# Kernel tuning notes

Measured on AMD Instinct MI355X. Metric: run time of the kernel, lower is better.

## Reference

```python
import jax, jax.numpy as jnp
import numpy as np

B, S, E, CS, NC, H = 4, 2048, 1024, 16, 8, 16
D = E + CS            # d_model = 1040
DH = D // H           # head_dim = 65
DFF = 4 * E           # forward_expansion * embed_size


def setup_inputs() -> dict:
    key = jax.random.key(0)
    ks = jax.random.split(key, 20)
    s = 0.02  # init scale for weights
    f32 = jnp.float32
    return {
        'x': jax.random.normal(ks[0], (B, S, E), f32),
        'conditioning': jax.random.uniform(ks[1], (B, S, CS), f32),
        # attention params (torch Linear convention: W is [out, in])
        'Wq': jax.random.normal(ks[2], (D, D), f32) * s,
        'bq': jnp.zeros((D,), f32),
        'Wv': jax.random.normal(ks[3], (D, D), f32) * s,
        'bv': jnp.zeros((D,), f32),
        'Wk': jax.random.normal(ks[4], (NC, D, D), f32) * s,  # stacked per-class key projections
        'bk': jnp.zeros((NC, D), f32),
        'Wo': jax.random.normal(ks[5], (D, D), f32) * s,
        'bo': jnp.zeros((D,), f32),
        # layernorms
        'g1': jnp.ones((E,), f32), 'bn1': jnp.zeros((E,), f32),
        'g2': jnp.ones((E,), f32), 'bn2': jnp.zeros((E,), f32),
        # feed-forward
        'Wf1': jax.random.normal(ks[6], (DFF, E), f32) * s,
        'bf1': jnp.zeros((DFF,), f32),
        'Wf2': jax.random.normal(ks[7], (E, DFF), f32) * s,
        'bf2': jnp.zeros((E,), f32),
    }


def _layernorm(x, g, b, eps=1e-5):
    m = jnp.mean(x, axis=-1, keepdims=True)
    v = jnp.mean(jnp.square(x - m), axis=-1, keepdims=True)
    return (x - m) * jax.lax.rsqrt(v + eps) * g + b


def reference(x, conditioning, Wq, bq, Wv, bv, Wk, bk, Wo, bo,
              g1, bn1, g2, bn2, Wf1, bf1, Wf2, bf2):
    # dropout is identity (eval mode)
    xn = _layernorm(x, g1, bn1)                       # [B,S,E]
    xc = jnp.concatenate([xn, conditioning], axis=-1)  # [B,S,D]

    q = (xc @ Wq.T + bq).reshape(B, S, H, DH).transpose(0, 2, 1, 3)  # [B,H,S,DH]
    v = (xc @ Wv.T + bv).reshape(B, S, H, DH).transpose(0, 2, 1, 3)

    # per-class keys: [B,C,S,D], then weighted-sum by conditioning[:,:,:NC]
    keys = jnp.einsum('bsd,cod->bcso', xc, Wk) + bk[None, :, None, :]
    w = conditioning[:, :, :NC]                        # [B,S,C]
    k = jnp.einsum('bsc,bcso->bso', w, keys)           # [B,S,D]
    k = k.reshape(B, S, H, DH).transpose(0, 2, 1, 3)   # [B,H,S,DH]

    scale = 1.0 / np.sqrt(DH).astype(np.float32)
    scores = jnp.einsum('bhqd,bhkd->bhqk', q, k) * scale
    attn = jax.nn.softmax(scores, axis=-1)
    o = jnp.einsum('bhqk,bhkd->bhqd', attn, v)
    o = o.transpose(0, 2, 1, 3).reshape(B, S, D)
    o = o @ Wo.T + bo

    h = xn + o[:, :, :E]                               # residual uses normed x
    ff = jnp.maximum(h @ Wf1.T + bf1, 0.0) @ Wf2.T + bf2
    return _layernorm(h + ff, g2, bn2)
```

## Files before the change

kernel.cpp:

```cpp
#include <hip/hip_runtime.h>
#include <hip/hip_bf16.h>
#include <math.h>

typedef __bf16 bf16;
typedef __bf16 v8bf __attribute__((ext_vector_type(8)));
typedef float v4f __attribute__((ext_vector_type(4)));

#define B_   4
#define S_   2048
#define E_   1024
#define CS_  16
#define NC_  8
#define H_   16
#define D_   1040
#define DH_  65
#define DFF_ 4096
#define M_   8192
#define KC_  1056
#define KH_  (4 * KC_)
#define KB2_ (8 * KC_)

__device__ __forceinline__ v4f mfma16(v8bf a, v8bf b, v4f c) {
    return __builtin_amdgcn_mfma_f32_16x16x32_bf16(a, b, c, 0, 0, 0);
}

__device__ __forceinline__ void async16(const bf16* g, bf16* l) {
    __builtin_amdgcn_global_load_lds(
        (const __attribute__((address_space(1))) unsigned int*)g,
        (__attribute__((address_space(3))) unsigned int*)l, 16, 0, 0);
}

__global__ __launch_bounds__(256) void k_cvt(const float* __restrict__ src,
                                             bf16* __restrict__ dst, int n) {
    int i = (blockIdx.x * 256 + threadIdx.x) * 4;
    if (i + 4 <= n) {
        float4 v = *(const float4*)(src + i);
        bf16 o[4] = {(bf16)v.x, (bf16)v.y, (bf16)v.z, (bf16)v.w};
        *(ushort4*)(dst + i) = *(const ushort4*)o;
    }
}

__global__ __launch_bounds__(256) void k_build_bk(const float* __restrict__ Wk,
                                                  bf16* __restrict__ Bp) {
    int c = blockIdx.y;
    int idx = blockIdx.x * 256 + threadIdx.x;
    if (idx >= 1040 * 130) return;
    int n = idx / 130, u = idx - n * 130;
    const float* src = Wk + ((size_t)(c * D_ + n)) * D_ + u * 8;
    float4 a = *(const float4*)src;
    float4 b = *(const float4*)(src + 4);
    bf16 o[8] = {(bf16)a.x, (bf16)a.y, (bf16)a.z, (bf16)a.w,
                 (bf16)b.x, (bf16)b.y, (bf16)b.z, (bf16)b.w};
    *(uint4*)(Bp + (size_t)n * KB2_ + c * KC_ + u * 8) = *(const uint4*)o;
}

__global__ __launch_bounds__(256) void k_scale_a(const bf16* __restrict__ xc,
                                                 const float* __restrict__ cond,
                                                 int coff, bf16* __restrict__ Ap) {
    int idx = blockIdx.x * 256 + threadIdx.x;
    int m = idx / 132, u = idx - m * 132;
    int j = u * 8;
    float4 w4 = *(const float4*)(cond + (size_t)m * CS_ + coff);
    float wv[4] = {w4.x, w4.y, w4.z, w4.w};
    bf16* dst = Ap + (size_t)m * KH_ + j;
    if (j < D_) {
        union { uint4 u4; bf16 h[8]; } src;
        src.u4 = *(const uint4*)(xc + (size_t)m * D_ + j);
        float xv[8];
#pragma unroll
        for (int e = 0; e < 8; ++e) xv[e] = (float)src.h[e];
#pragma unroll
        for (int cc = 0; cc < 4; ++cc) {
            bf16 o[8];
#pragma unroll
            for (int e = 0; e < 8; ++e) o[e] = (bf16)(xv[e] * wv[cc]);
            *(uint4*)(dst + cc * KC_) = *(const uint4*)o;
        }
    } else {
        uint4 z = {0u, 0u, 0u, 0u};
#pragma unroll
        for (int cc = 0; cc < 4; ++cc) *(uint4*)(dst + cc * KC_) = z;
    }
}

__global__ __launch_bounds__(256) void k_zero_pads(bf16* __restrict__ qp,
                                                   bf16* __restrict__ kp) {
    int i = blockIdx.x * 256 + threadIdx.x;
    int row = i >> 3, j = i & 7;
    uint4 z = {0u, 0u, 0u, 0u};
    bf16* base = (j < 4) ? qp : kp;
    ((uint4*)(base + (size_t)row * 96 + 64))[j & 3] = z;
}

__global__ __launch_bounds__(256) void k_ln_concat(
    const float* __restrict__ x, const float* __restrict__ cond,
    const float* __restrict__ g, const float* __restrict__ bn,
    bf16* __restrict__ xc)
{
    int row = blockIdx.x;
    int t = threadIdx.x;
    const float* xr = x + (size_t)row * E_;
    float4 v = *(const float4*)(xr + t * 4);
    float s = v.x + v.y + v.z + v.w;
    float ss = v.x * v.x + v.y * v.y + v.z * v.z + v.w * v.w;
#pragma unroll
    for (int off = 32; off; off >>= 1) {
        s  += __shfl_down(s, off);
        ss += __shfl_down(ss, off);
    }
    __shared__ float red[8];
    int wid = t >> 6;
    if ((t & 63) == 0) { red[wid] = s; red[4 + wid] = ss; }
    __syncthreads();
    float stot  = red[0] + red[1] + red[2] + red[3];
    float sstot = red[4] + red[5] + red[6] + red[7];
    float mean = stot * (1.0f / E_);
    float var  = sstot * (1.0f / E_) - mean * mean;
    float rs = rsqrtf(var + 1e-5f);
    bf16* xcr = xc + (size_t)row * D_;
    float vv[4] = {v.x, v.y, v.z, v.w};
#pragma unroll
    for (int j = 0; j < 4; ++j) {
        int i = t * 4 + j;
        xcr[i] = (bf16)(((vv[j] - mean) * rs) * g[i] + bn[i]);
    }
    if (t < CS_) xcr[E_ + t] = (bf16)cond[(size_t)row * CS_ + t];
}

__global__ __launch_bounds__(256) void k_gemm_k2(
    const bf16* __restrict__ A, const bf16* __restrict__ Bm,
    int koffB, bf16* __restrict__ Pout)
{
    __shared__ bf16 As[128][32];
    __shared__ bf16 Bs[128][32];
    int t = threadIdx.x;

    int pid = blockIdx.x;
    int gid = pid / 72;
    int rem = pid - gid * 72;
    int mi = gid * 8 + (rem & 7);
    int ni = rem >> 3;
    int m0 = mi << 7, n0 = ni << 7;

    int lane = t & 63, w = t >> 6;
    int wm = (w >> 1) * 64, wn = (w & 1) * 64;
    int lr = lane & 15, lq = lane >> 4;

    int row_i[2], seg_i[2];
#pragma unroll
    for (int i = 0; i < 2; ++i) { row_i[i] = (t + i * 256) >> 2; seg_i[i] = (t + i * 256) & 3; }

    v4f acc[4][4];
    v4f vzero = {0.f, 0.f, 0.f, 0.f};
#pragma unroll
    for (int mt = 0; mt < 4; ++mt)
#pragma unroll
        for (int nt = 0; nt < 4; ++nt) acc[mt][nt] = vzero;

    for (int kb = 0; kb < KH_ / 32; ++kb) {
        int k0 = kb << 5;
#pragma unroll
        for (int i = 0; i < 2; ++i) {
            async16(A + (size_t)(m0 + row_i[i]) * KH_ + k0 + seg_i[i] * 8,
                    &As[0][0] + (t + i * 256) * 8);
            async16(Bm + (size_t)(n0 + row_i[i]) * KB2_ + koffB + k0 + seg_i[i] * 8,
                    &Bs[0][0] + (t + i * 256) * 8);
        }
        __syncthreads();
        v8bf af[4], bfr[4];
#pragma unroll
        for (int mt = 0; mt < 4; ++mt) af[mt]  = *(const v8bf*)(&As[wm + mt * 16 + lr][lq * 8]);
#pragma unroll
        for (int nt = 0; nt < 4; ++nt) bfr[nt] = *(const v8bf*)(&Bs[wn + nt * 16 + lr][lq * 8]);
#pragma unroll
        for (int mt = 0; mt < 4; ++mt)
#pragma unroll
            for (int nt = 0; nt < 4; ++nt)
                acc[mt][nt] = mfma16(af[mt], bfr[nt], acc[mt][nt]);
        __syncthreads();
    }

#pragma unroll
    for (int mt = 0; mt < 4; ++mt)
#pragma unroll
        for (int reg = 0; reg < 4; ++reg) {
            int grow = m0 + wm + mt * 16 + lq * 4 + reg;
#pragma unroll
            for (int nt = 0; nt < 4; ++nt) {
                int gcol = n0 + wn + nt * 16 + lr;
                if (gcol < D_)
                    Pout[(size_t)grow * D_ + gcol] = (bf16)acc[mt][nt][reg];
            }
        }
}

__global__ __launch_bounds__(256) void k_comb_k(
    const bf16* __restrict__ P0, const bf16* __restrict__ P1,
    const float* __restrict__ condw, const float* __restrict__ bkp,
    bf16* __restrict__ kp)
{
    int idx = blockIdx.x * 256 + threadIdx.x;
    int m = idx / 1040, n = idx - m * 1040;
    float v = (float)P0[idx] + (float)P1[idx];
#pragma unroll
    for (int c = 0; c < NC_; ++c)
        v += condw[(size_t)m * CS_ + c] * bkp[(size_t)c * D_ + n];
    int h = n / 65, d = n - h * 65;
    int b = m >> 11, s = m & 2047;
    kp[(((size_t)(b * 16 + h)) * S_ + s) * 96 + d] = (bf16)v;
}

#define EP_QV  0
#define EP_O   1
#define EP_FF1 2
#define EP_FF2 3

template<int EP>
__global__ __launch_bounds__(256) void k_gemm(
    const bf16* __restrict__ A, const bf16* __restrict__ Bm,
    const float* __restrict__ bias, const float* __restrict__ bias2,
    int M, int N, int K, int lda, int ldb, int nbn,
    bf16* __restrict__ Cb, float* __restrict__ Cf, int ldc,
    const bf16* __restrict__ res, int ldres, bf16* __restrict__ Cb2)
{
    __shared__ bf16 As[128][32];
    __shared__ bf16 Bs[128][32];
    int t = threadIdx.x;

    int pid = blockIdx.x;
    int nig = 8 * nbn;
    int gid = pid / nig;
    int rem = pid - gid * nig;
    int mi = gid * 8 + (rem & 7);
    int ni = rem >> 3;
    int m0 = mi << 7, n0 = ni << 7;

    int lane = t & 63, w = t >> 6;
    int wm = (w >> 1) * 64, wn = (w & 1) * 64;
    int lr = lane & 15, lq = lane >> 4;

    int row_i[2], seg_i[2];
#pragma unroll
    for (int i = 0; i < 2; ++i) { row_i[i] = (t + i * 256) >> 2; seg_i[i] = (t + i * 256) & 3; }

    v4f acc[4][4];
    v4f vzero = {0.f, 0.f, 0.f, 0.f};
#pragma unroll
    for (int mt = 0; mt < 4; ++mt)
#pragma unroll
        for (int nt = 0; nt < 4; ++nt) acc[mt][nt] = vzero;

    const int KF = K >> 5;
    const bool KR = (K & 31) != 0;

    for (int kb = 0; kb < KF; ++kb) {
        int k0 = kb << 5;
#pragma unroll
        for (int i = 0; i < 2; ++i) {
            async16(A + (size_t)(m0 + row_i[i]) * lda + k0 + seg_i[i] * 8,
                    &As[0][0] + (t + i * 256) * 8);
            async16(Bm + (size_t)(n0 + row_i[i]) * ldb + k0 + seg_i[i] * 8,
                    &Bs[0][0] + (t + i * 256) * 8);
        }
        __syncthreads();
        v8bf af[4], bfr[4];
#pragma unroll
        for (int mt = 0; mt < 4; ++mt) af[mt]  = *(const v8bf*)(&As[wm + mt * 16 + lr][lq * 8]);
#pragma unroll
        for (int nt = 0; nt < 4; ++nt) bfr[nt] = *(const v8bf*)(&Bs[wn + nt * 16 + lr][lq * 8]);
#pragma unroll
        for (int mt = 0; mt < 4; ++mt)
#pragma unroll
            for (int nt = 0; nt < 4; ++nt)
                acc[mt][nt] = mfma16(af[mt], bfr[nt], acc[mt][nt]);
        __syncthreads();
    }
    if (KR) {
        int k0 = KF << 5;
#pragma unroll
        for (int i = 0; i < 2; ++i) {
            int gk = k0 + seg_i[i] * 8;
            uint4 val = {0u, 0u, 0u, 0u};
            if (gk + 8 <= K) val = *(const uint4*)(A + (size_t)(m0 + row_i[i]) * lda + gk);
            *(uint4*)(&As[row_i[i]][seg_i[i] * 8]) = val;
            uint4 bv = {0u, 0u, 0u, 0u};
            int gn = n0 + row_i[i];
            if (gn < N && gk + 8 <= K) bv = *(const uint4*)(Bm + (size_t)gn * ldb + gk);
            *(uint4*)(&Bs[row_i[i]][seg_i[i] * 8]) = bv;
        }
        __syncthreads();
        v8bf af[4], bfr[4];
#pragma unroll
        for (int mt = 0; mt < 4; ++mt) af[mt]  = *(const v8bf*)(&As[wm + mt * 16 + lr][lq * 8]);
#pragma unroll
        for (int nt = 0; nt < 4; ++nt) bfr[nt] = *(const v8bf*)(&Bs[wn + nt * 16 + lr][lq * 8]);
#pragma unroll
        for (int mt = 0; mt < 4; ++mt)
#pragma unroll
            for (int nt = 0; nt < 4; ++nt)
                acc[mt][nt] = mfma16(af[mt], bfr[nt], acc[mt][nt]);
        __syncthreads();
    }

#pragma unroll
    for (int mt = 0; mt < 4; ++mt) {
#pragma unroll
        for (int reg = 0; reg < 4; ++reg) {
            int grow = m0 + wm + mt * 16 + lq * 4 + reg;
#pragma unroll
            for (int nt = 0; nt < 4; ++nt) {
                int gcol = n0 + wn + nt * 16 + lr;
                float vacc = acc[mt][nt][reg];
                if constexpr (EP == EP_QV) {
                    if (gcol < D_) {
                        float o = (vacc + bias[gcol]) * 0.1789442960f;
                        int h = gcol / 65, d = gcol - h * 65;
                        int b = grow >> 11, s = grow & 2047;
                        Cb[(((size_t)(b * 16 + h)) * S_ + s) * 96 + d] = (bf16)o;
                    } else if (gcol < 2 * D_) {
                        int col = gcol - D_;
                        Cb2[(size_t)grow * D_ + col] = (bf16)(vacc + bias2[col]);
                    }
                } else if constexpr (EP == EP_O) {
                    float o = vacc + bias[gcol] + (float)res[(size_t)grow * ldres + gcol];
                    Cb[(size_t)grow * ldc + gcol] = (bf16)o;
                } else if constexpr (EP == EP_FF1) {
                    float o = vacc + bias[gcol];
                    Cb[(size_t)grow * ldc + gcol] = (bf16)fmaxf(o, 0.f);
                } else {
                    Cf[(size_t)grow * ldc + gcol] =
                        vacc + bias[gcol] + (float)res[(size_t)grow * ldres + gcol];
                }
            }
        }
    }
}

__global__ __launch_bounds__(256) void k_transpose_v(
    const bf16* __restrict__ v, bf16* __restrict__ vt)
{
    int bh = blockIdx.y, s0 = blockIdx.x * 64;
    int b = bh >> 4, h = bh & 15;
    __shared__ bf16 tile[80][65];
#pragma unroll
    for (int i = 0; i < 20; ++i) {
        int idx = threadIdx.x + i * 256;
        int d = idx % 80, sl = idx / 80;
        bf16 val = (bf16)0.f;
        if (d < DH_) val = v[((size_t)b * S_ + s0 + sl) * D_ + h * DH_ + d];
        tile[d][sl] = val;
    }
    __syncthreads();
#pragma unroll
    for (int i = 0; i < 20; ++i) {
        int idx = threadIdx.x + i * 256;
        int sl = idx % 64, d = idx / 64;
        vt[((size_t)bh * 80 + d) * S_ + s0 + sl] = tile[d][sl];
    }
}

__global__ __launch_bounds__(256) void k_attn(
    const bf16* __restrict__ qp, const bf16* __restrict__ kp,
    const bf16* __restrict__ vt, bf16* __restrict__ o)
{
    int bh = blockIdx.y;
    int s0 = blockIdx.x * 64;
    int b = bh >> 4, h = bh & 15;
    int t = threadIdx.x, lane = t & 63, w = t >> 6;
    int lr = lane & 15, lq = lane >> 4;

    __shared__ bf16 Kbuf[2][64 * 96];
    __shared__ bf16 Psh[4][16 * 72];
    bf16* Ps = Psh[w];
    bf16* k0p = &Kbuf[0][0];

    const bf16* qbase = qp + ((size_t)bh * S_ + s0 + w * 16 + lr) * 96;
    v8bf qreg[3];
#pragma unroll
    for (int ks = 0; ks < 3; ++ks)
        qreg[ks] = *(const v8bf*)(qbase + ks * 32 + lq * 8);

    const bf16* kpb = kp + (size_t)bh * S_ * 96;
    const bf16* vbase = vt + ((size_t)bh * 80 + lr) * S_ + lq * 8;

#pragma unroll
    for (int i = 0; i < 3; ++i)
        async16(kpb + (t + i * 256) * 8, k0p + (t + i * 256) * 8);

    float m_s = -1e30f, l_s = 0.f;
    v4f o_acc[5];
    v4f vzero = {0.f, 0.f, 0.f, 0.f};
#pragma unroll
    for (int nt = 0; nt < 5; ++nt) o_acc[nt] = vzero;

    __syncthreads();

    int cur = 0;
    for (int kb = 0; kb < S_ / 64; ++kb) {
        const bf16* Kc = k0p + cur * (64 * 96);
        if (kb + 1 < S_ / 64) {
            bf16* Kn = k0p + (cur ^ 1) * (64 * 96);
            const bf16* src = kpb + (size_t)(kb + 1) * (64 * 96);
#pragma unroll
            for (int i = 0; i < 3; ++i)
                async16(src + (t + i * 256) * 8, Kn + (t + i * 256) * 8);
        }

        v4f sacc[4];
#pragma unroll
        for (int kt = 0; kt < 4; ++kt) sacc[kt] = vzero;
        __builtin_amdgcn_s_setprio(1);
#pragma unroll
        for (int ks = 0; ks < 3; ++ks)
#pragma unroll
            for (int kt = 0; kt < 4; ++kt) {
                v8bf kf = *(const v8bf*)(Kc + (kt * 16 + lr) * 96 + ks * 32 + lq * 8);
                sacc[kt] = mfma16(kf, qreg[ks], sacc[kt]);
            }
        __builtin_amdgcn_s_setprio(0);

        v8bf vf0[5], vf1[5];
        const bf16* vb0 = vbase + kb * 64;
#pragma unroll
        for (int nt = 0; nt < 5; ++nt) vf0[nt] = *(const v8bf*)(vb0 + nt * 16 * S_);
#pragma unroll
        for (int nt = 0; nt < 5; ++nt) vf1[nt] = *(const v8bf*)(vb0 + nt * 16 * S_ + 32);

        float mx = sacc[0][0];
#pragma unroll
        for (int kt = 0; kt < 4; ++kt)
#pragma unroll
            for (int r = 0; r < 4; ++r) mx = fmaxf(mx, sacc[kt][r]);
        mx = fmaxf(mx, __shfl_xor(mx, 16));
        mx = fmaxf(mx, __shfl_xor(mx, 32));
        float mnew = fmaxf(m_s, mx);
        float alpha = __builtin_amdgcn_exp2f(m_s - mnew);
        float ps = 0.f;
#pragma unroll
        for (int kt = 0; kt < 4; ++kt) {
            bf16 p4[4];
#pragma unroll
            for (int r = 0; r < 4; ++r) {
                float p = __builtin_amdgcn_exp2f(sacc[kt][r] - mnew);
                ps += p;
                p4[r] = (bf16)p;
            }
            *(uint2*)(&Ps[lr * 72 + kt * 16 + lq * 4]) = *(const uint2*)p4;
        }
        ps += __shfl_xor(ps, 16);
        ps += __shfl_xor(ps, 32);
        l_s = l_s * alpha + ps;
        m_s = mnew;

#pragma unroll
        for (int nt = 0; nt < 5; ++nt)
#pragma unroll
            for (int r = 0; r < 4; ++r) o_acc[nt][r] *= alpha;

        asm volatile("s_waitcnt lgkmcnt(0)" ::: "memory");

        __builtin_amdgcn_s_setprio(1);
        {
            v8bf pf0 = *(const v8bf*)(&Ps[lr * 72 + lq * 8]);
            v8bf pf1 = *(const v8bf*)(&Ps[lr * 72 + 32 + lq * 8]);
#pragma unroll
            for (int nt = 0; nt < 5; ++nt) o_acc[nt] = mfma16(vf0[nt], pf0, o_acc[nt]);
#pragma unroll
            for (int nt = 0; nt < 5; ++nt) o_acc[nt] = mfma16(vf1[nt], pf1, o_acc[nt]);
        }
        __builtin_amdgcn_s_setprio(0);
        __syncthreads();
        cur ^= 1;
    }

    float inv = 1.0f / l_s;
    bf16* obase = o + (size_t)(b * S_ + s0 + w * 16 + lr) * D_ + h * DH_;
#pragma unroll
    for (int nt = 0; nt < 4; ++nt)
#pragma unroll
        for (int r = 0; r < 4; ++r)
            obase[nt * 16 + lq * 4 + r] = (bf16)(o_acc[nt][r] * inv);
    if (lq == 0) obase[64] = (bf16)(o_acc[4][0] * inv);
}

__global__ __launch_bounds__(256) void k_ln_out(
    const float* __restrict__ z, const float* __restrict__ g,
    const float* __restrict__ bn, float* __restrict__ out)
{
    int row = blockIdx.x;
    int t = threadIdx.x;
    const float* zr = z + (size_t)row * E_;
    float4 v = *(const float4*)(zr + t * 4);
    float s = v.x + v.y + v.z + v.w;
    float ss = v.x * v.x + v.y * v.y + v.z * v.z + v.w * v.w;
#pragma unroll
    for (int off = 32; off; off >>= 1) {
        s  += __shfl_down(s, off);
        ss += __shfl_down(ss, off);
    }
    __shared__ float red[8];
    int wid = t >> 6;
    if ((t & 63) == 0) { red[wid] = s; red[4 + wid] = ss; }
    __syncthreads();
    float stot  = red[0] + red[1] + red[2] + red[3];
    float sstot = red[4] + red[5] + red[6] + red[7];
    float mean = stot * (1.0f / E_);
    float var  = sstot * (1.0f / E_) - mean * mean;
    float rs = rsqrtf(var + 1e-5f);
    float* outr = out + (size_t)row * E_;
    float vv[4] = {v.x, v.y, v.z, v.w};
#pragma unroll
    for (int j = 0; j < 4; ++j) {
        int i = t * 4 + j;
        outr[i] = ((vv[j] - mean) * rs) * g[i] + bn[i];
    }
}

extern "C" void kernel_launch(void* const* d_in, const int* in_sizes, int n_in,
                              void* d_out, int out_size, void* d_ws, size_t ws_size,
                              hipStream_t stream) {
    const float* x    = (const float*)d_in[0];
    const float* cond = (const float*)d_in[1];
    const float* Wq   = (const float*)d_in[2];
    const float* bq   = (const float*)d_in[3];
    const float* Wv   = (const float*)d_in[4];
    const float* bv   = (const float*)d_in[5];
    const float* Wk   = (const float*)d_in[6];
    const float* bk   = (const float*)d_in[7];
    const float* Wo   = (const float*)d_in[8];
    const float* bo   = (const float*)d_in[9];
    const float* g1   = (const float*)d_in[10];
    const float* bn1  = (const float*)d_in[11];
    const float* g2   = (const float*)d_in[12];
    const float* bn2  = (const float*)d_in[13];
    const float* Wf1  = (const float*)d_in[14];
    const float* bf1  = (const float*)d_in[15];
    const float* Wf2  = (const float*)d_in[16];
    const float* bf2  = (const float*)d_in[17];
    float* out = (float*)d_out;

    char* ws = (char*)d_ws;
    bf16* Wqv_b = (bf16*)(ws + 0);
    bf16* Wo_b  = (bf16*)(ws + 4526080);
    bf16* Wf1_b = (bf16*)(ws + 6656000);
    bf16* Wf2_b = (bf16*)(ws + 15044608);
    bf16*  xc   = (bf16*)(ws + 23433216);
    bf16*  Bpk  = (bf16*)(ws + 40472576);
    bf16*  Apk  = (bf16*)(ws + 59936768);
    bf16*  P0k  = (bf16*)(ws + 129142784);
    bf16*  P1k  = (bf16*)(ws + 146182144);
    bf16*  qp   = (bf16*)(ws + 40472576);
    bf16*  kp   = (bf16*)(ws + 65638400);
    bf16*  vb   = (bf16*)(ws + 90804224);
    bf16*  hb   = (bf16*)(ws + 90804224);
    bf16*  vtb  = (bf16*)(ws + 107843584);
    bf16*  ob   = (bf16*)(ws + 128815104);
    bf16*  ff1  = (bf16*)(ws + 23433216);
    float* zb   = (float*)(ws + 107843584);

    k_cvt<<<(1081600 / 4 + 255) / 256, 256, 0, stream>>>(Wq, Wqv_b, 1081600);
    k_cvt<<<(1081600 / 4 + 255) / 256, 256, 0, stream>>>(Wv, Wqv_b + 1081600, 1081600);
    k_cvt<<<(1064960 / 4 + 255) / 256, 256, 0, stream>>>(Wo, Wo_b, 1064960);
    k_cvt<<<(4194304 / 4 + 255) / 256, 256, 0, stream>>>(Wf1, Wf1_b, 4194304);
    k_cvt<<<(4194304 / 4 + 255) / 256, 256, 0, stream>>>(Wf2, Wf2_b, 4194304);

    k_ln_concat<<<M_, 256, 0, stream>>>(x, cond, g1, bn1, xc);

    k_build_bk<<<dim3((1040 * 130 + 255) / 256, 8), 256, 0, stream>>>(Wk, Bpk);
    k_scale_a<<<(M_ * 132) / 256, 256, 0, stream>>>(xc, cond, 0, Apk);
    k_gemm_k2<<<576, 256, 0, stream>>>(Apk, Bpk, 0, P0k);
    k_scale_a<<<(M_ * 132) / 256, 256, 0, stream>>>(xc, cond, 4, Apk);
    k_gemm_k2<<<576, 256, 0, stream>>>(Apk, Bpk, KH_, P1k);

    k_zero_pads<<<4096, 256, 0, stream>>>(qp, kp);
    k_comb_k<<<(M_ * D_) / 256, 256, 0, stream>>>(P0k, P1k, cond, bk, kp);

    k_gemm<EP_QV><<<64 * 17, 256, 0, stream>>>(xc, Wqv_b, bq, bv, M_, 2 * D_, D_, D_, D_, 17,
                                               qp, nullptr, 0, nullptr, 0, vb);

    k_transpose_v<<<dim3(S_ / 64, 64), 256, 0, stream>>>(vb, vtb);
    k_attn<<<dim3(S_ / 64, 64), 256, 0, stream>>>(qp, kp, vtb, ob);

    k_gemm<EP_O><<<64 * 8, 256, 0, stream>>>(ob, Wo_b, bo, nullptr, M_, E_, D_, D_, D_, 8,
                                             hb, nullptr, E_, xc, D_, nullptr);
    k_gemm<EP_FF1><<<64 * 32, 256, 0, stream>>>(hb, Wf1_b, bf1, nullptr, M_, DFF_, E_, E_, E_, 32,
                                                ff1, nullptr, DFF_, nullptr, 0, nullptr);
    k_gemm<EP_FF2><<<64 * 8, 256, 0, stream>>>(ff1, Wf2_b, bf2, nullptr, M_, E_, DFF_, DFF_, DFF_, 8,
                                               nullptr, zb, E_, hb, E_, nullptr);

    k_ln_out<<<M_, 256, 0, stream>>>(zb, g2, bn2, out);
}
```

Measured before the change: 1.123 ms.

## Process two query tiles per attention block, stage V in LDS with XOR swizzle

Measured after the change: 958.9 us. 14.6% less time.

```diff
diff --git a/kernel.cpp b/kernel.cpp
--- a/kernel.cpp
+++ b/kernel.cpp
@@ -207,7 +207,8 @@
         v += condw[(size_t)m * CS_ + c] * bkp[(size_t)c * D_ + n];
     int h = n / 65, d = n - h * 65;
     int b = m >> 11, s = m & 2047;
-    kp[(((size_t)(b * 16 + h)) * S_ + s) * 96 + d] = (bf16)v;
+    int d2 = (d < 64) ? (d ^ ((s & 7) << 3)) : (d ^ ((s & 3) << 3));
+    kp[(((size_t)(b * 16 + h)) * S_ + s) * 96 + d2] = (bf16)v;
 }
 
 #define EP_QV  0
@@ -355,7 +356,8 @@
     for (int i = 0; i < 20; ++i) {
         int idx = threadIdx.x + i * 256;
         int sl = idx % 64, d = idx / 64;
-        vt[((size_t)bh * 80 + d) * S_ + s0 + sl] = tile[d][sl];
+        int sl2 = sl ^ ((d & 7) << 3);
+        vt[((size_t)bh * 80 + d) * S_ + s0 + sl2] = tile[d][sl];
     }
 }
 
@@ -364,123 +366,185 @@
     const bf16* __restrict__ vt, bf16* __restrict__ o)
 {
     int bh = blockIdx.y;
-    int s0 = blockIdx.x * 64;
+    int s0 = blockIdx.x * 128;
     int b = bh >> 4, h = bh & 15;
     int t = threadIdx.x, lane = t & 63, w = t >> 6;
     int lr = lane & 15, lq = lane >> 4;
 
     __shared__ bf16 Kbuf[2][64 * 96];
+    __shared__ bf16 Vbuf[2][80 * 64];
     __shared__ bf16 Psh[4][16 * 72];
     bf16* Ps = Psh[w];
-    bf16* k0p = &Kbuf[0][0];
-
-    const bf16* qbase = qp + ((size_t)bh * S_ + s0 + w * 16 + lr) * 96;
-    v8bf qreg[3];
-#pragma unroll
-    for (int ks = 0; ks < 3; ++ks)
-        qreg[ks] = *(const v8bf*)(qbase + ks * 32 + lq * 8);
+
+    v8bf qreg[2][3];
+#pragma unroll
+    for (int fq = 0; fq < 2; ++fq) {
+        const bf16* qbase = qp + ((size_t)bh * S_ + s0 + fq * 64 + w * 16 + lr) * 96;
+#pragma unroll
+        for (int ks = 0; ks < 3; ++ks)
+            qreg[fq][ks] = *(const v8bf*)(qbase + ks * 32 + lq * 8);
+    }
 
     const bf16* kpb = kp + (size_t)bh * S_ * 96;
-    const bf16* vbase = vt + ((size_t)bh * 80 + lr) * S_ + lq * 8;
+    const bf16* vpb = vt + (size_t)bh * 80 * S_;
+
+    int vidx[3]; bool vact[3];
+#pragma unroll
+    for (int i = 0; i < 3; ++i) { vidx[i] = t + i * 256; vact[i] = vidx[i] < 640; }
 
 #pragma unroll
     for (int i = 0; i < 3; ++i)
-        async16(kpb + (t + i * 256) * 8, k0p + (t + i * 256) * 8);
-
-    float m_s = -1e30f, l_s = 0.f;
-    v4f o_acc[5];
+        async16(kpb + (size_t)(t + i * 256) * 8, &Kbuf[0][(t + i * 256) * 8]);
+#pragma unroll
+    for (int i = 0; i < 3; ++i)
+        if (vact[i])
+            async16(vpb + (size_t)(vidx[i] >> 3) * S_ + (vidx[i] & 7) * 8, &Vbuf[0][vidx[i] * 8]);
+
+    float m_0 = -1e30f, l_0 = 0.f, m_1 = -1e30f, l_1 = 0.f;
+    v4f oa0[5], oa1[5];
     v4f vzero = {0.f, 0.f, 0.f, 0.f};
 #pragma unroll
-    for (int nt = 0; nt < 5; ++nt) o_acc[nt] = vzero;
+    for (int nt = 0; nt < 5; ++nt) { oa0[nt] = vzero; oa1[nt] = vzero; }
+
+    int swA = (lr & 7) << 3;
+    int swB = (lr & 3) << 3;
 
     __syncthreads();
 
     int cur = 0;
     for (int kb = 0; kb < S_ / 64; ++kb) {
-        const bf16* Kc = k0p + cur * (64 * 96);
         if (kb + 1 < S_ / 64) {
-            bf16* Kn = k0p + (cur ^ 1) * (64 * 96);
-            const bf16* src = kpb + (size_t)(kb + 1) * (64 * 96);
+            const bf16* ksrc = kpb + (size_t)(kb + 1) * (64 * 96);
+            bf16* Kn = &Kbuf[cur ^ 1][0];
+            bf16* Vn = &Vbuf[cur ^ 1][0];
 #pragma unroll
             for (int i = 0; i < 3; ++i)
-                async16(src + (t + i * 256) * 8, Kn + (t + i * 256) * 8);
-        }
-
-        v4f sacc[4];
-#pragma unroll
-        for (int kt = 0; kt < 4; ++kt) sacc[kt] = vzero;
+                async16(ksrc + (size_t)(t + i * 256) * 8, Kn + (t + i * 256) * 8);
+#pragma unroll
+            for (int i = 0; i < 3; ++i)
+                if (vact[i])
+                    async16(vpb + (size_t)(vidx[i] >> 3) * S_ + (kb + 1) * 64 + (vidx[i] & 7) * 8,
+                            Vn + vidx[i] * 8);
+        }
+        const bf16* Kc = &Kbuf[cur][0];
+        const bf16* Vc = &Vbuf[cur][0];
+
+        v4f s0acc[4], s1acc[4];
+#pragma unroll
+        for (int kt = 0; kt < 4; ++kt) { s0acc[kt] = vzero; s1acc[kt] = vzero; }
         __builtin_amdgcn_s_setprio(1);
 #pragma unroll
-        for (int ks = 0; ks < 3; ++ks)
+        for (int ks = 0; ks < 3; ++ks) {
+            int cb = (ks * 32 + lq * 8) ^ (ks == 2 ? swB : swA);
 #pragma unroll
             for (int kt = 0; kt < 4; ++kt) {
-                v8bf kf = *(const v8bf*)(Kc + (kt * 16 + lr) * 96 + ks * 32 + lq * 8);
-                sacc[kt] = mfma16(kf, qreg[ks], sacc[kt]);
+                v8bf kf = *(const v8bf*)(Kc + (kt * 16 + lr) * 96 + cb);
+                s0acc[kt] = mfma16(kf, qreg[0][ks], s0acc[kt]);
+                s1acc[kt] = mfma16(kf, qreg[1][ks], s1acc[kt]);
             }
+        }
         __builtin_amdgcn_s_setprio(0);
 
-        v8bf vf0[5], vf1[5];
-        const bf16* vb0 = vbase + kb * 64;
-#pragma unroll
-        for (int nt = 0; nt < 5; ++nt) vf0[nt] = *(const v8bf*)(vb0 + nt * 16 * S_);
-#pragma unroll
-        for (int nt = 0; nt < 5; ++nt) vf1[nt] = *(const v8bf*)(vb0 + nt * 16 * S_ + 32);
-
-        float mx = sacc[0][0];
+        float a0;
+        {
+            float mx = s0acc[0][0];
+#pragma unroll
+            for (int kt = 0; kt < 4; ++kt)
+#pragma unroll
+                for (int r = 0; r < 4; ++r) mx = fmaxf(mx, s0acc[kt][r]);
+            mx = fmaxf(mx, __shfl_xor(mx, 16));
+            mx = fmaxf(mx, __shfl_xor(mx, 32));
+            float mnew = fmaxf(m_0, mx);
+            a0 = __builtin_amdgcn_exp2f(m_0 - mnew);
+            float ps = 0.f;
+#pragma unroll
+            for (int kt = 0; kt < 4; ++kt) {
+                union { bf16 h[4]; uint2 v; } p4;
+#pragma unroll
+                for (int r = 0; r < 4; ++r) {
+                    float p = __builtin_amdgcn_exp2f(s0acc[kt][r] - mnew);
+                    ps += p;
+                    p4.h[r] = (bf16)p;
+                }
+                *(uint2*)(&Ps[lr * 72 + kt * 16 + lq * 4]) = p4.v;
+            }
+            ps += __shfl_xor(ps, 16);
+            ps += __shfl_xor(ps, 32);
+            l_0 = l_0 * a0 + ps;
+            m_0 = mnew;
+        }
+        uint2 p1p[4];
+        float a1;
+        {
+            float mx = s1acc[0][0];
+#pragma unroll
+            for (int kt = 0; kt < 4; ++kt)
+#pragma unroll
+                for (int r = 0; r < 4; ++r) mx = fmaxf(mx, s1acc[kt][r]);
+            mx = fmaxf(mx, __shfl_xor(mx, 16));
+            mx = fmaxf(mx, __shfl_xor(mx, 32));
+            float mnew = fmaxf(m_1, mx);
+            a1 = __builtin_amdgcn_exp2f(m_1 - mnew);
+            float ps = 0.f;
+#pragma unroll
+            for (int kt = 0; kt < 4; ++kt) {
+                union { bf16 h[4]; uint2 v; } p4;
+#pragma unroll
+                for (int r = 0; r < 4; ++r) {
+                    float p = __builtin_amdgcn_exp2f(s1acc[kt][r] - mnew);
+                    ps += p;
+                    p4.h[r] = (bf16)p;
+                }
+                p1p[kt] = p4.v;
+            }
+            ps += __shfl_xor(ps, 16);
+            ps += __shfl_xor(ps, 32);
+            l_1 = l_1 * a1 + ps;
+            m_1 = mnew;
+        }
+
+        v8bf pf0[2], pf1[2];
+        pf0[0] = *(const v8bf*)(&Ps[lr * 72 + lq * 8]);
+        pf0[1] = *(const v8bf*)(&Ps[lr * 72 + 32 + lq * 8]);
 #pragma unroll
         for (int kt = 0; kt < 4; ++kt)
-#pragma unroll
-            for (int r = 0; r < 4; ++r) mx = fmaxf(mx, sacc[kt][r]);
-        mx = fmaxf(mx, __shfl_xor(mx, 16));
-        mx = fmaxf(mx, __shfl_xor(mx, 32));
-        float mnew = fmaxf(m_s, mx);
-        float alpha = __builtin_amdgcn_exp2f(m_s - mnew);
-        float ps = 0.f;
-#pragma unroll
-        for (int kt = 0; kt < 4; ++kt) {
-            bf16 p4[4];
-#pragma unroll
-            for (int r = 0; r < 4; ++r) {
-                float p = __builtin_amdgcn_exp2f(sacc[kt][r] - mnew);
-                ps += p;
-                p4[r] = (bf16)p;
+            *(uint2*)(&Ps[lr * 72 + kt * 16 + lq * 4]) = p1p[kt];
+        pf1[0] = *(const v8bf*)(&Ps[lr * 72 + lq * 8]);
+        pf1[1] = *(const v8bf*)(&Ps[lr * 72 + 32 + lq * 8]);
+
+#pragma unroll
+        for (int nt = 0; nt < 5; ++nt)
+#pragma unroll
+            for (int r = 0; r < 4; ++r) { oa0[nt][r] *= a0; oa1[nt][r] *= a1; }
+
+        __builtin_amdgcn_s_setprio(1);
+#pragma unroll
+        for (int kt2 = 0; kt2 < 2; ++kt2) {
+            int vb2 = (kt2 * 32 + lq * 8) ^ swA;
+#pragma unroll
+            for (int nt = 0; nt < 5; ++nt) {
+                v8bf vf = *(const v8bf*)(Vc + (nt * 16 + lr) * 64 + vb2);
+                oa0[nt] = mfma16(vf, pf0[kt2], oa0[nt]);
+                oa1[nt] = mfma16(vf, pf1[kt2], oa1[nt]);
             }
-            *(uint2*)(&Ps[lr * 72 + kt * 16 + lq * 4]) = *(const uint2*)p4;
-        }
-        ps += __shfl_xor(ps, 16);
-        ps += __shfl_xor(ps, 32);
-        l_s = l_s * alpha + ps;
-        m_s = mnew;
-
-#pragma unroll
-        for (int nt = 0; nt < 5; ++nt)
-#pragma unroll
-            for (int r = 0; r < 4; ++r) o_acc[nt][r] *= alpha;
-
-        asm volatile("s_waitcnt lgkmcnt(0)" ::: "memory");
-
-        __builtin_amdgcn_s_setprio(1);
-        {
-            v8bf pf0 = *(const v8bf*)(&Ps[lr * 72 + lq * 8]);
-            v8bf pf1 = *(const v8bf*)(&Ps[lr * 72 + 32 + lq * 8]);
-#pragma unroll
-            for (int nt = 0; nt < 5; ++nt) o_acc[nt] = mfma16(vf0[nt], pf0, o_acc[nt]);
-#pragma unroll
-            for (int nt = 0; nt < 5; ++nt) o_acc[nt] = mfma16(vf1[nt], pf1, o_acc[nt]);
         }
         __builtin_amdgcn_s_setprio(0);
         __syncthreads();
         cur ^= 1;
     }
 
-    float inv = 1.0f / l_s;
-    bf16* obase = o + (size_t)(b * S_ + s0 + w * 16 + lr) * D_ + h * DH_;
-#pragma unroll
-    for (int nt = 0; nt < 4; ++nt)
-#pragma unroll
-        for (int r = 0; r < 4; ++r)
-            obase[nt * 16 + lq * 4 + r] = (bf16)(o_acc[nt][r] * inv);
-    if (lq == 0) obase[64] = (bf16)(o_acc[4][0] * inv);
+#pragma unroll
+    for (int fq = 0; fq < 2; ++fq) {
+        float inv = 1.0f / (fq ? l_1 : l_0);
+        const v4f* oa = fq ? oa1 : oa0;
+        bf16* obase = o + (size_t)(b * S_ + s0 + fq * 64 + w * 16 + lr) * D_ + h * DH_;
+#pragma unroll
+        for (int nt = 0; nt < 4; ++nt)
+#pragma unroll
+            for (int r = 0; r < 4; ++r)
+                obase[nt * 16 + lq * 4 + r] = (bf16)(oa[nt][r] * inv);
+        if (lq == 0) obase[64] = (bf16)(oa[4][0] * inv);
+    }
 }
 
 __global__ __launch_bounds__(256) void k_ln_out(
@@ -579,7 +643,7 @@
                                                qp, nullptr, 0, nullptr, 0, vb);
 
     k_transpose_v<<<dim3(S_ / 64, 64), 256, 0, stream>>>(vb, vtb);
-    k_attn<<<dim3(S_ / 64, 64), 256, 0, stream>>>(qp, kp, vtb, ob);
+    k_attn<<<dim3(S_ / 128, 64), 256, 0, stream>>>(qp, kp, vtb, ob);
 
     k_gemm<EP_O><<<64 * 8, 256, 0, stream>>>(ob, Wo_b, bo, nullptr, M_, E_, D_, D_, D_, 8,
                                              hb, nullptr, E_, xc, D_, nullptr);
```
